# Kernel optimization log

Measured on AMD Instinct MI355X. Metric: run time of the kernel, lower is better.

Reference implementation:

```python
import jax, jax.numpy as jnp
import numpy as np

N = 50000        # num nodes
NFEAT = 512      # input feature dim
NCLASS = 256     # output classes (out_features of out_att)
E_RAND = 800000  # random edges; + N self-loops
NEG_SLOPE = 0.2  # leakyrelu alpha


def setup_inputs() -> dict:
    key = jax.random.key(0)
    k1, k2, k3, k4 = jax.random.split(key, 4)
    x = jax.random.normal(k1, (N, NFEAT), dtype=jnp.float32)
    W = jax.random.normal(k2, (NFEAT, NCLASS), dtype=jnp.float32) / np.float32(np.sqrt(NFEAT))
    a = jax.random.normal(k3, (2 * NCLASS,), dtype=jnp.float32) / np.float32(np.sqrt(2 * NCLASS))
    rand_edges = jax.random.randint(k4, (2, E_RAND), 0, N, dtype=jnp.int32)
    self_loops = jnp.tile(jnp.arange(N, dtype=jnp.int32), (2, 1))
    edge_index = jnp.concatenate([rand_edges, self_loops], axis=1)  # [2, E]
    return {"x": x, "W": W, "a": a, "edge_index": edge_index}


def reference(x, W, a, edge_index):
    # Eval-mode SpGAT: dropout is identity (training=False).
    row, col = edge_index[0], edge_index[1]  # edge = adj.nonzero().t(): row aggregates from col
    h = x @ W                                # [N, F]
    F_out = h.shape[1]
    # a @ cat(h[row], h[col]) == (h @ a1)[row] + (h @ a2)[col]  (avoids [E, 2F] concat)
    s_row = h @ a[:F_out]                    # [N]
    s_col = h @ a[F_out:]                    # [N]
    logits = s_row[row] + s_col[col]         # [E]
    e = jnp.exp(-jax.nn.leaky_relu(logits, negative_slope=NEG_SLOPE))  # [E]
    rowsum = jax.ops.segment_sum(e, row, num_segments=N)               # [N]
    msgs = e[:, None] * h[col]                                         # [E, F]
    h_prime = jax.ops.segment_sum(msgs, row, num_segments=N) / rowsum[:, None]
    return jax.nn.log_softmax(jax.nn.elu(h_prime), axis=1)
```

## Files before the change

kernel.cpp:

```cpp
#include <hip/hip_runtime.h>
#include <math.h>

#define NNODES   50000
#define NFEAT    512
#define NCLASS   256
#define NEG_SLOPE 0.2f
#define MPAD     50048
#define GBLK     391

typedef __attribute__((ext_vector_type(8))) short short8;
typedef __attribute__((ext_vector_type(4))) float floatx4;

__device__ __forceinline__ unsigned short f2bf(float f) {
    unsigned u = __builtin_bit_cast(unsigned, f);
    u += 0x7fffu + ((u >> 16) & 1u);
    return (unsigned short)(u >> 16);
}
__device__ __forceinline__ float bf2f(unsigned short s) {
    return __builtin_bit_cast(float, ((unsigned)s) << 16);
}
__device__ __forceinline__ float bf2f_lo(unsigned u) {
    return __builtin_bit_cast(float, u << 16);
}
__device__ __forceinline__ float bf2f_hi(unsigned u) {
    return __builtin_bit_cast(float, u & 0xffff0000u);
}
__device__ __forceinline__ unsigned pack_bf16_rh(float lo, float hi) {
    const unsigned ulo = __builtin_bit_cast(unsigned, lo) + 0x8000u;
    const unsigned uhi = __builtin_bit_cast(unsigned, hi) + 0x8000u;
    return __builtin_amdgcn_perm(uhi, ulo, 0x07060302);
}

#if __has_builtin(__builtin_amdgcn_fdot2_f32_bf16)
#define HAVE_DOT2 1
typedef __attribute__((ext_vector_type(2))) __bf16 bfx2;
__device__ __forceinline__ float dot2bf(unsigned hpair, unsigned epair, float acc) {
    return __builtin_amdgcn_fdot2_f32_bf16(__builtin_bit_cast(bfx2, hpair),
                                           __builtin_bit_cast(bfx2, epair), acc, false);
}
#endif

__global__ __launch_bounds__(256) void init_kernel(const float* __restrict__ W,
                                                   unsigned short* __restrict__ Wt,
                                                   int* __restrict__ zero2, int zn) {
    const int i = blockIdx.x * 256 + threadIdx.x;
    const int n = i >> 9;
    const int k = i & 511;
    Wt[i] = f2bf(W[(size_t)k * NCLASS + n]);
    for (int j = i; j < zn; j += 131072) zero2[j] = 0;
}

__global__ __launch_bounds__(256, 2) void gemm_mfma_kernel(const float* __restrict__ x,
                                                           const unsigned short* __restrict__ Wt,
                                                           unsigned short* __restrict__ hb,
                                                           const float* __restrict__ a,
                                                           float* __restrict__ s_row,
                                                           float* __restrict__ s_col,
                                                           const int* __restrict__ erow,
                                                           int* __restrict__ deg,
                                                           int M, int E) {
    __shared__ union {
        struct { short As[128 * 32]; short Bs[256 * 32]; } k;
        short Cs[32 * 260];
    } u;

    const int tid  = threadIdx.x;
    const int w    = tid >> 6;
    const int lane = tid & 63;
    const int rowbase = blockIdx.x * 128;

    const int wm = w & 1;
    const int wn = w >> 1;
    const int srow = lane >> 2;
    const int skq  = (lane & 3) << 3;
    const int fm = lane & 15;
    const int fq = lane >> 4;

    floatx4 acc[4][8];
#pragma unroll
    for (int i = 0; i < 4; ++i)
#pragma unroll
        for (int j = 0; j < 8; ++j)
            acc[i][j] = (floatx4){0.f, 0.f, 0.f, 0.f};

    for (int k0 = 0; k0 < NFEAT; k0 += 32) {
#pragma unroll
        for (int t = 0; t < 4; ++t) {
            const int seg = w * 4 + t;
            const int nr  = seg * 16 + srow;
            __builtin_amdgcn_global_load_lds(
                (const __attribute__((address_space(1))) void*)(Wt + (size_t)nr * NFEAT + k0 + skq),
                (__attribute__((address_space(3))) void*)(u.k.Bs + seg * 512), 16, 0, 0);
        }
#pragma unroll
        for (int t = 0; t < 2; ++t) {
            const int seg = w * 2 + t;
            const int rr  = seg * 16 + srow;
            const int ar  = min(rowbase + rr, M - 1);
            const float4* xp = (const float4*)&x[(size_t)ar * NFEAT + k0 + skq];
            const float4 u0 = xp[0];
            const float4 u1 = xp[1];
            uint4 o;
            o.x = pack_bf16_rh(u0.x, u0.y);
            o.y = pack_bf16_rh(u0.z, u0.w);
            o.z = pack_bf16_rh(u1.x, u1.y);
            o.w = pack_bf16_rh(u1.z, u1.w);
            *(uint4*)&u.k.As[rr * 32 + skq] = o;
        }
        __syncthreads();

        short8 af[4];
#pragma unroll
        for (int mt = 0; mt < 4; ++mt)
            af[mt] = *(const short8*)&u.k.As[(wm * 64 + mt * 16 + fm) * 32 + fq * 8];
#pragma unroll
        for (int nt = 0; nt < 8; ++nt) {
            const short8 bfr = *(const short8*)&u.k.Bs[(wn * 128 + nt * 16 + fm) * 32 + fq * 8];
#pragma unroll
            for (int mt = 0; mt < 4; ++mt)
                acc[mt][nt] = __builtin_amdgcn_mfma_f32_16x16x32_bf16(af[mt], bfr, acc[mt][nt], 0, 0, 0);
        }
        __syncthreads();
    }

#pragma unroll
    for (int p = 0; p < 4; ++p) {
        __syncthreads();
        if ((w & 1) == (p >> 1)) {
#pragma unroll
            for (int mt2 = 0; mt2 < 2; ++mt2) {
                const int mt = (p & 1) * 2 + mt2;
#pragma unroll
                for (int nt = 0; nt < 8; ++nt)
#pragma unroll
                    for (int r = 0; r < 4; ++r)
                        u.Cs[(mt2 * 16 + fq * 4 + r) * 260 + wn * 128 + nt * 16 + fm] =
                            (short)f2bf(acc[mt][nt][r]);
            }
        }
        __syncthreads();
#pragma unroll
        for (int k = 0; k < 8; ++k) {
            const int idx = tid + k * 256;
            const int lrow = idx >> 6;
            const int c4 = (idx & 63) << 2;
            const int grow = rowbase + p * 32 + lrow;
            const uint2 vv = *(const uint2*)&u.Cs[lrow * 260 + c4];
            const float f0 = bf2f_lo(vv.x), f1 = bf2f_hi(vv.x);
            const float f2 = bf2f_lo(vv.y), f3 = bf2f_hi(vv.y);
            const float4 A1 = *(const float4*)&a[c4];
            const float4 A2 = *(const float4*)&a[NCLASS + c4];
            float p1 = f0 * A1.x + f1 * A1.y + f2 * A1.z + f3 * A1.w;
            float p2 = f0 * A2.x + f1 * A2.y + f2 * A2.z + f3 * A2.w;
#pragma unroll
            for (int off = 1; off < 64; off <<= 1) {
                p1 += __shfl_xor(p1, off);
                p2 += __shfl_xor(p2, off);
            }
            if (grow < M) {
                *(uint2*)&hb[(size_t)grow * NCLASS + c4] = vv;
                if (lane == 0) {
                    s_row[grow] = p1;
                    s_col[grow] = p2;
                }
            }
        }
    }

    const int gtid = blockIdx.x * 256 + tid;
    for (int i = gtid; i < E; i += GBLK * 256)
        atomicAdd(&deg[erow[i]], 1);
}

__global__ __launch_bounds__(256) void scan1_kernel(const int* __restrict__ deg,
                                                    int* __restrict__ tmp,
                                                    int* __restrict__ blocksum, int n) {
    __shared__ int buf[256];
    const int i = blockIdx.x * 256 + threadIdx.x;
    const int t = threadIdx.x;
    buf[t] = (i < n) ? deg[i] : 0;
    __syncthreads();
#pragma unroll
    for (int off = 1; off < 256; off <<= 1) {
        const int uv = (t >= off) ? buf[t - off] : 0;
        __syncthreads();
        buf[t] += uv;
        __syncthreads();
    }
    if (i < n) tmp[i] = buf[t];
    if (t == 255) blocksum[blockIdx.x] = buf[255];
}

__global__ __launch_bounds__(256) void scan3_kernel(const int* __restrict__ tmp,
                                                    const int* __restrict__ blocksum,
                                                    int* __restrict__ rowstart, int n, int nb) {
    __shared__ int buf[256];
    const int t = threadIdx.x;
    buf[t] = (t < nb) ? blocksum[t] : 0;
    __syncthreads();
#pragma unroll
    for (int off = 1; off < 256; off <<= 1) {
        const int uv = (t >= off) ? buf[t - off] : 0;
        __syncthreads();
        buf[t] += uv;
        __syncthreads();
    }
    const int boff = (blockIdx.x == 0) ? 0 : buf[blockIdx.x - 1];
    const int i = blockIdx.x * 256 + t;
    if (i < n) rowstart[i + 1] = tmp[i] + boff;
    if (i == 0) rowstart[0] = 0;
}

__global__ __launch_bounds__(256) void scatter_kernel(const int* __restrict__ row,
                                                      const int* __restrict__ col,
                                                      const float* __restrict__ s_row,
                                                      const float* __restrict__ s_col,
                                                      const int* __restrict__ rowstart,
                                                      int* __restrict__ cursor,
                                                      int2* __restrict__ sorted_ce, int e) {
    const int i = blockIdx.x * 256 + threadIdx.x;
    if (i >= e) return;
    const int r = row[i];
    const int c = col[i];
    const float logit = s_row[r] + s_col[c];
    const float lr = logit > 0.f ? logit : NEG_SLOPE * logit;
    const float ew = __expf(-lr);
    const int pos = atomicAdd(&cursor[r], 1);
    int2 v;
    v.x = c;
    v.y = __builtin_bit_cast(int, ew);
    sorted_ce[rowstart[r] + pos] = v;
}

__global__ __launch_bounds__(256) void aggregate_kernel(const unsigned short* __restrict__ hb,
                                                        const int2* __restrict__ sorted_ce,
                                                        const int* __restrict__ rowstart,
                                                        float* __restrict__ out, int n) {
    const int wave = (int)((blockIdx.x * (size_t)blockDim.x + threadIdx.x) >> 6);
    const int lane = threadIdx.x & 63;
    if (wave >= n) return;
    const int r = wave;
    const int jb = rowstart[r];
    const int je = rowstart[r + 1];
    const int fo = lane << 2;

    float rowsum = 0.f;
    int j = jb;

#ifdef HAVE_DOT2
    float ac0 = 0.f, ac1 = 0.f, ac2 = 0.f, ac3 = 0.f;
    for (; j + 3 < je; j += 4) {
        const int2 v0 = sorted_ce[j];
        const int2 v1 = sorted_ce[j + 1];
        const int2 v2 = sorted_ce[j + 2];
        const int2 v3 = sorted_ce[j + 3];
        const uint2 g0 = *(const uint2*)&hb[(size_t)v0.x * NCLASS + fo];
        const uint2 g1 = *(const uint2*)&hb[(size_t)v1.x * NCLASS + fo];
        const uint2 g2 = *(const uint2*)&hb[(size_t)v2.x * NCLASS + fo];
        const uint2 g3 = *(const uint2*)&hb[(size_t)v3.x * NCLASS + fo];
        const float e0 = __builtin_bit_cast(float, v0.y);
        const float e1 = __builtin_bit_cast(float, v1.y);
        const float e2 = __builtin_bit_cast(float, v2.y);
        const float e3 = __builtin_bit_cast(float, v3.y);
        const unsigned ep01 = pack_bf16_rh(e0, e1);
        const unsigned ep23 = pack_bf16_rh(e2, e3);
        rowsum += (e0 + e1) + (e2 + e3);
        ac0 = dot2bf(__builtin_amdgcn_perm(g1.x, g0.x, 0x05040100), ep01, ac0);
        ac1 = dot2bf(__builtin_amdgcn_perm(g1.x, g0.x, 0x07060302), ep01, ac1);
        ac2 = dot2bf(__builtin_amdgcn_perm(g1.y, g0.y, 0x05040100), ep01, ac2);
        ac3 = dot2bf(__builtin_amdgcn_perm(g1.y, g0.y, 0x07060302), ep01, ac3);
        ac0 = dot2bf(__builtin_amdgcn_perm(g3.x, g2.x, 0x05040100), ep23, ac0);
        ac1 = dot2bf(__builtin_amdgcn_perm(g3.x, g2.x, 0x07060302), ep23, ac1);
        ac2 = dot2bf(__builtin_amdgcn_perm(g3.y, g2.y, 0x05040100), ep23, ac2);
        ac3 = dot2bf(__builtin_amdgcn_perm(g3.y, g2.y, 0x07060302), ep23, ac3);
    }
    float4 acc = make_float4(ac0, ac1, ac2, ac3);
#else
    float4 acc = make_float4(0.f, 0.f, 0.f, 0.f);
    for (; j + 3 < je; j += 4) {
        const int2 v0 = sorted_ce[j];
        const int2 v1 = sorted_ce[j + 1];
        const int2 v2 = sorted_ce[j + 2];
        const int2 v3 = sorted_ce[j + 3];
        const uint2 g0 = *(const uint2*)&hb[(size_t)v0.x * NCLASS + fo];
        const uint2 g1 = *(const uint2*)&hb[(size_t)v1.x * NCLASS + fo];
        const uint2 g2 = *(const uint2*)&hb[(size_t)v2.x * NCLASS + fo];
        const uint2 g3 = *(const uint2*)&hb[(size_t)v3.x * NCLASS + fo];
        const float e0 = __builtin_bit_cast(float, v0.y);
        const float e1 = __builtin_bit_cast(float, v1.y);
        const float e2 = __builtin_bit_cast(float, v2.y);
        const float e3 = __builtin_bit_cast(float, v3.y);
        rowsum += (e0 + e1) + (e2 + e3);
        acc.x += e0 * bf2f_lo(g0.x) + e1 * bf2f_lo(g1.x) + e2 * bf2f_lo(g2.x) + e3 * bf2f_lo(g3.x);
        acc.y += e0 * bf2f_hi(g0.x) + e1 * bf2f_hi(g1.x) + e2 * bf2f_hi(g2.x) + e3 * bf2f_hi(g3.x);
        acc.z += e0 * bf2f_lo(g0.y) + e1 * bf2f_lo(g1.y) + e2 * bf2f_lo(g2.y) + e3 * bf2f_lo(g3.y);
        acc.w += e0 * bf2f_hi(g0.y) + e1 * bf2f_hi(g1.y) + e2 * bf2f_hi(g2.y) + e3 * bf2f_hi(g3.y);
    }
#endif
    for (; j < je; ++j) {
        const int2 v = sorted_ce[j];
        const uint2 g = *(const uint2*)&hb[(size_t)v.x * NCLASS + fo];
        const float e = __builtin_bit_cast(float, v.y);
        rowsum += e;
        acc.x += e * bf2f_lo(g.x);
        acc.y += e * bf2f_hi(g.x);
        acc.z += e * bf2f_lo(g.y);
        acc.w += e * bf2f_hi(g.y);
    }

    const float inv = 1.f / rowsum;
    float v[4] = {acc.x * inv, acc.y * inv, acc.z * inv, acc.w * inv};
#pragma unroll
    for (int i = 0; i < 4; ++i)
        v[i] = v[i] > 0.f ? v[i] : __expf(v[i]) - 1.f;

    float m = fmaxf(fmaxf(v[0], v[1]), fmaxf(v[2], v[3]));
#pragma unroll
    for (int off = 32; off > 0; off >>= 1) m = fmaxf(m, __shfl_xor(m, off));
    float s = 0.f;
#pragma unroll
    for (int i = 0; i < 4; ++i) s += __expf(v[i] - m);
#pragma unroll
    for (int off = 32; off > 0; off >>= 1) s += __shfl_xor(s, off);
    const float lse = m + __logf(s);

    float4 o = make_float4(v[0] - lse, v[1] - lse, v[2] - lse, v[3] - lse);
    *(float4*)&out[(size_t)r * NCLASS + fo] = o;
}

extern "C" void kernel_launch(void* const* d_in, const int* in_sizes, int n_in,
                              void* d_out, int out_size, void* d_ws, size_t ws_size,
                              hipStream_t stream) {
    const float* x  = (const float*)d_in[0];
    const float* W  = (const float*)d_in[1];
    const float* a  = (const float*)d_in[2];
    const int* edge = (const int*)d_in[3];
    float* out = (float*)d_out;

    const int M = in_sizes[0] / NFEAT;
    const int E = in_sizes[3] / 2;
    const int* row = edge;
    const int* col = edge + E;

    char* ws = (char*)d_ws;
    size_t off = 0;
    auto carve = [&](size_t bytes) -> char* {
        char* p = ws + off;
        off = (off + bytes + 255) & ~(size_t)255;
        return p;
    };
    unsigned short* Wt = (unsigned short*)carve((size_t)NCLASS * NFEAT * sizeof(short));
    unsigned short* hb = (unsigned short*)carve((size_t)M * NCLASS * sizeof(short));
    int*   zero2    = (int*)carve((size_t)2 * M * sizeof(int));
    int*   deg      = zero2;
    int*   cursor   = zero2 + M;
    float* s_row    = (float*)carve((size_t)M * sizeof(float));
    float* s_col    = (float*)carve((size_t)M * sizeof(float));
    int*   rowstart = (int*)carve((size_t)(M + 1) * sizeof(int));
    int*   tmp_scan = (int*)carve((size_t)M * sizeof(int));
    int*   blocksum = (int*)carve((size_t)256 * sizeof(int));
    int2*  sorted_ce = (int2*)carve((size_t)E * sizeof(int2));

    init_kernel<<<512, 256, 0, stream>>>(W, Wt, zero2, 2 * M);

    gemm_mfma_kernel<<<GBLK, 256, 0, stream>>>(x, Wt, hb, a, s_row, s_col, row, deg, M, E);

    const int nb1 = (M + 255) / 256;
    scan1_kernel<<<nb1, 256, 0, stream>>>(deg, tmp_scan, blocksum, M);
    scan3_kernel<<<nb1, 256, 0, stream>>>(tmp_scan, blocksum, rowstart, M, nb1);
    scatter_kernel<<<(E + 255) / 256, 256, 0, stream>>>(row, col, s_row, s_col,
                                                        rowstart, cursor, sorted_ce, E);

    aggregate_kernel<<<(M + 3) / 4, 256, 0, stream>>>(hb, sorted_ce, rowstart, out, M);
}
```

Baseline: 322.2 us.

## Double-buffer GEMM LDS tiles and halve block rows for higher occupancy

The projection GEMM now uses 64-row tiles instead of 128, doubling the grid and raising the launch-bounds occupancy hint from 2 to 4 blocks per CU. It also double-buffers the A and B LDS tiles, prefetching the next k-slice of x and W while MFMAs run on the current one, which drops one barrier per iteration. The aim is to hide global-load latency and improve CU utilisation. The cost is more LDS per block, more blocks re-reading W, and register pressure under the tighter launch bound.

New measurement: 325.3 us. No clear change (+1.0%).

```diff
diff --git a/kernel.cpp b/kernel.cpp
--- a/kernel.cpp
+++ b/kernel.cpp
@@ -6,7 +6,7 @@
 #define NCLASS   256
 #define NEG_SLOPE 0.2f
 #define MPAD     50048
-#define GBLK     391
+#define GBLK     782
 
 typedef __attribute__((ext_vector_type(8))) short short8;
 typedef __attribute__((ext_vector_type(4))) float floatx4;
@@ -50,7 +50,7 @@
     for (int j = i; j < zn; j += 131072) zero2[j] = 0;
 }
 
-__global__ __launch_bounds__(256, 2) void gemm_mfma_kernel(const float* __restrict__ x,
+__global__ __launch_bounds__(256, 4) void gemm_mfma_kernel(const float* __restrict__ x,
                                                            const unsigned short* __restrict__ Wt,
                                                            unsigned short* __restrict__ hb,
                                                            const float* __restrict__ a,
@@ -60,14 +60,14 @@
                                                            int* __restrict__ deg,
                                                            int M, int E) {
     __shared__ union {
-        struct { short As[128 * 32]; short Bs[256 * 32]; } k;
+        struct { short As[2][64 * 32]; short Bs[2][256 * 32]; } k;
         short Cs[32 * 260];
     } u;
 
     const int tid  = threadIdx.x;
     const int w    = tid >> 6;
     const int lane = tid & 63;
-    const int rowbase = blockIdx.x * 128;
+    const int rowbase = blockIdx.x * 64;
 
     const int wm = w & 1;
     const int wn = w >> 1;
@@ -76,67 +76,91 @@
     const int fm = lane & 15;
     const int fq = lane >> 4;
 
-    floatx4 acc[4][8];
-#pragma unroll
-    for (int i = 0; i < 4; ++i)
+    floatx4 acc[2][8];
+#pragma unroll
+    for (int i = 0; i < 2; ++i)
 #pragma unroll
         for (int j = 0; j < 8; ++j)
             acc[i][j] = (floatx4){0.f, 0.f, 0.f, 0.f};
 
+    const int arow = min(rowbase + w * 16 + srow, M - 1);
+    const size_t abase = (size_t)arow * NFEAT + skq;
+    const int lrowA = (w * 16 + srow) * 32 + skq;
+
+#define STAGE_B(buf, k0)                                                                      \
+    {                                                                                         \
+        _Pragma("unroll")                                                                     \
+        for (int t = 0; t < 4; ++t) {                                                         \
+            const int seg = w * 4 + t;                                                        \
+            const int nr  = seg * 16 + srow;                                                  \
+            __builtin_amdgcn_global_load_lds(                                                 \
+                (const __attribute__((address_space(1))) void*)(Wt + (size_t)nr * NFEAT + (k0) + skq), \
+                (__attribute__((address_space(3))) void*)(&u.k.Bs[buf][seg * 512]), 16, 0, 0); \
+        }                                                                                     \
+    }
+
+    STAGE_B(0, 0)
+    {
+        const float4* xp = (const float4*)&x[abase];
+        const float4 u0 = xp[0];
+        const float4 u1 = xp[1];
+        uint4 o;
+        o.x = pack_bf16_rh(u0.x, u0.y);
+        o.y = pack_bf16_rh(u0.z, u0.w);
+        o.z = pack_bf16_rh(u1.x, u1.y);
+        o.w = pack_bf16_rh(u1.z, u1.w);
+        *(uint4*)&u.k.As[0][lrowA] = o;
+    }
+    __syncthreads();
+
+    int cur = 0;
     for (int k0 = 0; k0 < NFEAT; k0 += 32) {
-#pragma unroll
-        for (int t = 0; t < 4; ++t) {
-            const int seg = w * 4 + t;
-            const int nr  = seg * 16 + srow;
-            __builtin_amdgcn_global_load_lds(
-                (const __attribute__((address_space(1))) void*)(Wt + (size_t)nr * NFEAT + k0 + skq),
-                (__attribute__((address_space(3))) void*)(u.k.Bs + seg * 512), 16, 0, 0);
-        }
-#pragma unroll
-        for (int t = 0; t < 2; ++t) {
-            const int seg = w * 2 + t;
-            const int rr  = seg * 16 + srow;
-            const int ar  = min(rowbase + rr, M - 1);
-            const float4* xp = (const float4*)&x[(size_t)ar * NFEAT + k0 + skq];
-            const float4 u0 = xp[0];
-            const float4 u1 = xp[1];
+        const int nxt = cur ^ 1;
+        const bool have_next = (k0 + 32) < NFEAT;
+        float4 p0, p1;
+        if (have_next) {
+            const float4* xp = (const float4*)&x[abase + k0 + 32];
+            p0 = xp[0];
+            p1 = xp[1];
+            STAGE_B(nxt, k0 + 32)
+        }
+
+        short8 af[2];
+#pragma unroll
+        for (int mt = 0; mt < 2; ++mt)
+            af[mt] = *(const short8*)&u.k.As[cur][(wm * 32 + mt * 16 + fm) * 32 + fq * 8];
+#pragma unroll
+        for (int nt = 0; nt < 8; ++nt) {
+            const short8 bfr = *(const short8*)&u.k.Bs[cur][(wn * 128 + nt * 16 + fm) * 32 + fq * 8];
+#pragma unroll
+            for (int mt = 0; mt < 2; ++mt)
+                acc[mt][nt] = __builtin_amdgcn_mfma_f32_16x16x32_bf16(af[mt], bfr, acc[mt][nt], 0, 0, 0);
+        }
+
+        if (have_next) {
             uint4 o;
-            o.x = pack_bf16_rh(u0.x, u0.y);
-            o.y = pack_bf16_rh(u0.z, u0.w);
-            o.z = pack_bf16_rh(u1.x, u1.y);
-            o.w = pack_bf16_rh(u1.z, u1.w);
-            *(uint4*)&u.k.As[rr * 32 + skq] = o;
-        }
-        __syncthreads();
-
-        short8 af[4];
-#pragma unroll
-        for (int mt = 0; mt < 4; ++mt)
-            af[mt] = *(const short8*)&u.k.As[(wm * 64 + mt * 16 + fm) * 32 + fq * 8];
-#pragma unroll
-        for (int nt = 0; nt < 8; ++nt) {
-            const short8 bfr = *(const short8*)&u.k.Bs[(wn * 128 + nt * 16 + fm) * 32 + fq * 8];
-#pragma unroll
-            for (int mt = 0; mt < 4; ++mt)
-                acc[mt][nt] = __builtin_amdgcn_mfma_f32_16x16x32_bf16(af[mt], bfr, acc[mt][nt], 0, 0, 0);
-        }
-        __syncthreads();
-    }
-
-#pragma unroll
-    for (int p = 0; p < 4; ++p) {
-        __syncthreads();
-        if ((w & 1) == (p >> 1)) {
-#pragma unroll
-            for (int mt2 = 0; mt2 < 2; ++mt2) {
-                const int mt = (p & 1) * 2 + mt2;
+            o.x = pack_bf16_rh(p0.x, p0.y);
+            o.y = pack_bf16_rh(p0.z, p0.w);
+            o.z = pack_bf16_rh(p1.x, p1.y);
+            o.w = pack_bf16_rh(p1.z, p1.w);
+            *(uint4*)&u.k.As[nxt][lrowA] = o;
+        }
+        __syncthreads();
+        cur = nxt;
+    }
+
+#pragma unroll
+    for (int p = 0; p < 2; ++p) {
+        __syncthreads();
+        if (wm == p) {
+#pragma unroll
+            for (int mt = 0; mt < 2; ++mt)
 #pragma unroll
                 for (int nt = 0; nt < 8; ++nt)
 #pragma unroll
                     for (int r = 0; r < 4; ++r)
-                        u.Cs[(mt2 * 16 + fq * 4 + r) * 260 + wn * 128 + nt * 16 + fm] =
+                        u.Cs[(mt * 16 + fq * 4 + r) * 260 + wn * 128 + nt * 16 + fm] =
                             (short)f2bf(acc[mt][nt][r]);
-            }
         }
         __syncthreads();
 #pragma unroll
```
